# Kernel optimization log

Hardware: AMD Instinct MI355X
Metric: run time of the kernel (lower is better)

Reference implementation:

```python
import jax, jax.numpy as jnp
import numpy as np
from jax import lax

DIM = 128
HEADS = 8
HEAD_DIM = DIM // HEADS
SR = 2
B, H, W = 2, 80, 80
SCALE = HEAD_DIM ** (-0.5)
BN_EPS = 1e-5


def _conv1x1(x, w, b):
    # x: (B,C,H,W), w: (O,C), b: (O,)
    return jnp.einsum('bchw,oc->bohw', x, w) + b[None, :, None, None]


def setup_inputs() -> dict:
    key = jax.random.key(0)
    ks = jax.random.split(key, 12)
    s = DIM ** -0.5
    x = jax.random.normal(ks[0], (B, DIM, H, W), dtype=jnp.float32)
    q_w = jax.random.normal(ks[1], (DIM, DIM), dtype=jnp.float32) * s
    q_b = jnp.zeros((DIM,), jnp.float32)
    k_w = jax.random.normal(ks[2], (DIM, DIM), dtype=jnp.float32) * s
    k_b = jnp.zeros((DIM,), jnp.float32)
    v_w = jax.random.normal(ks[3], (DIM, DIM), dtype=jnp.float32) * s
    v_b = jnp.zeros((DIM,), jnp.float32)
    sr_w = jax.random.normal(ks[4], (DIM, DIM, SR, SR), dtype=jnp.float32) * (s / SR)
    sr_b = jnp.zeros((DIM,), jnp.float32)
    bn_gamma = jnp.ones((DIM,), jnp.float32)
    bn_beta = jnp.zeros((DIM,), jnp.float32)
    bn_mean = jnp.zeros((DIM,), jnp.float32)
    bn_var = jnp.ones((DIM,), jnp.float32)
    proj_w = jax.random.normal(ks[5], (DIM, DIM), dtype=jnp.float32) * s
    proj_b = jnp.zeros((DIM,), jnp.float32)
    return dict(x=x, q_w=q_w, q_b=q_b, k_w=k_w, k_b=k_b, v_w=v_w, v_b=v_b,
                sr_w=sr_w, sr_b=sr_b, bn_gamma=bn_gamma, bn_beta=bn_beta,
                bn_mean=bn_mean, bn_var=bn_var, proj_w=proj_w, proj_b=proj_b)


def reference(x, q_w, q_b, k_w, k_b, v_w, v_b, sr_w, sr_b,
              bn_gamma, bn_beta, bn_mean, bn_var, proj_w, proj_b):
    b, c, h, w = x.shape
    n = h * w
    # q: (B,h,N,d)
    q = _conv1x1(x, q_w, q_b).reshape(b, HEADS, HEAD_DIM, n).transpose(0, 1, 3, 2)
    # spatial reduction: Conv2d(k=SR, s=SR) + BN(eval) + ReLU
    x_kv = lax.conv_general_dilated(x, sr_w, window_strides=(SR, SR),
                                    padding='VALID',
                                    dimension_numbers=('NCHW', 'OIHW', 'NCHW'))
    x_kv = x_kv + sr_b[None, :, None, None]
    inv = bn_gamma / jnp.sqrt(bn_var + BN_EPS)
    x_kv = x_kv * inv[None, :, None, None] + (bn_beta - bn_mean * inv)[None, :, None, None]
    x_kv = jax.nn.relu(x_kv)
    n_kv = x_kv.shape[2] * x_kv.shape[3]
    k = _conv1x1(x_kv, k_w, k_b).reshape(b, HEADS, HEAD_DIM, n_kv).transpose(0, 1, 3, 2)
    v = _conv1x1(x_kv, v_w, v_b).reshape(b, HEADS, HEAD_DIM, n_kv).transpose(0, 1, 3, 2)
    # explicit attention: (B,h,N,N_kv)
    attn = jnp.einsum('bhnd,bhmd->bhnm', q, k) * SCALE
    attn = jax.nn.softmax(attn, axis=-1)
    out = jnp.einsum('bhnm,bhmd->bhnd', attn, v)  # (B,h,N,d)
    # faithful to source layout: transpose(1,2) then reshape to (B,C,H,W)
    out = out.transpose(0, 2, 1, 3).reshape(b, c, h, w)
    out = _conv1x1(out, proj_w, proj_b)
    return out
```

## Files before the change

kernel.cpp:

```cpp
#include <hip/hip_runtime.h>
#include <hip/hip_bf16.h>
#include <cmath>

#define DIM 128
#define HEADS 8
#define NBATCH 2
#define NQ 6400
#define NKV 1600
#define NC 50
#define NSPLIT 5
#define CPS 10
#define BN_EPS 1e-5f
#define LOG2E 1.4426950408889634f

typedef __bf16 bf16_t;
typedef __attribute__((ext_vector_type(8))) __bf16 bf16x8;
typedef __attribute__((ext_vector_type(16))) float f32x16;

union BF8U { bf16x8 v; unsigned u[4]; };

__device__ inline unsigned packbf2(float a, float b) {
  union { __hip_bfloat162 v; unsigned u; } r;
  r.v = __float22bfloat162_rn(make_float2(a, b));
  return r.u;
}

__device__ inline unsigned short f2bf(float v) {
  unsigned u = __float_as_uint(v);
  return (unsigned short)((u + 0x7FFFu + ((u >> 16) & 1u)) >> 16);
}

__global__ __launch_bounds__(256) void wcast(
    const float* __restrict__ qw, const float* __restrict__ kw,
    const float* __restrict__ vw, const float* __restrict__ pw,
    const float* __restrict__ srw, unsigned short* __restrict__ Wb)
{
  int e4 = (blockIdx.x * 256 + threadIdx.x) * 4;
  const float* src; int idx;
  if (e4 < 16384)      { src = qw;  idx = e4; }
  else if (e4 < 32768) { src = kw;  idx = e4 - 16384; }
  else if (e4 < 49152) { src = vw;  idx = e4 - 32768; }
  else if (e4 < 65536) { src = pw;  idx = e4 - 49152; }
  else                 { src = srw; idx = e4 - 65536; }
  float4 v = *(const float4*)(src + idx);
  uint2 wv;
  wv.x = packbf2(v.x, v.y);
  wv.y = packbf2(v.z, v.w);
  *(uint2*)&Wb[e4] = wv;
}

__global__ __launch_bounds__(256) void mgemm_qsrkv(
    const float* __restrict__ x, const bf16_t* __restrict__ Wb,
    const float* __restrict__ q_b, const float* __restrict__ sr_b,
    const float* __restrict__ k_b, const float* __restrict__ v_b,
    const float* __restrict__ bng, const float* __restrict__ bnb,
    const float* __restrict__ bnm, const float* __restrict__ bnv,
    unsigned short* __restrict__ Qb,
    unsigned short* __restrict__ Kp, unsigned short* __restrict__ Vp,
    float sl)
{
  __shared__ __align__(16) unsigned short xs4[32][520];
  __shared__ __align__(16) unsigned short xs[32][136];
  int t = threadIdx.x;
  int ln = t & 31, hf = (t >> 5) & 1, wid = t >> 6;
  int b = blockIdx.y;
  int o = wid * 32 + ln;

  if (blockIdx.x < 50) {
    int cid = blockIdx.x;
    int s0 = cid * 32;

    {
      int tx = t & 31, g = t >> 5;
      int s = s0 + tx;
      int i = s / 40, j = s % 40;
      const float* xb = x + (size_t)b * DIM * NQ;
#pragma unroll
      for (int u = 0; u < 32; ++u) {
        int idx2 = g * 32 + u;
        int c = idx2 >> 1, ky = idx2 & 1;
        const float* src = xb + (size_t)c * NQ + (2 * i + ky) * 80 + 2 * j;
        float2 vv = *(const float2*)src;
        *(unsigned*)&xs4[tx][c * 4 + ky * 2] = packbf2(vv.x, vv.y);
      }
    }
    __syncthreads();

    const unsigned short* arow = &xs4[ln][hf * 8];
    const bf16_t* brow = &Wb[65536 + (size_t)o * 512 + hf * 8];
    f32x16 acc = {};
#pragma unroll 8
    for (int c0 = 0; c0 < 512; c0 += 16) {
      bf16x8 af = *(const bf16x8*)&arow[c0];
      bf16x8 bf = *(const bf16x8*)&brow[c0];
      acc = __builtin_amdgcn_mfma_f32_32x32x16_bf16(af, bf, acc, 0, 0, 0);
    }
    float bv = sr_b[o];
    float inv = bng[o] / sqrtf(bnv[o] + BN_EPS);
    float b2 = bnb[o] - bnm[o] * inv;
#pragma unroll
    for (int g = 0; g < 4; ++g)
#pragma unroll
      for (int jj = 0; jj < 4; ++jj) {
        int sr = 8 * g + 4 * hf + jj;
        xs[sr][o] = f2bf(fmaxf((acc[4 * g + jj] + bv) * inv + b2, 0.f));
      }
    __syncthreads();

    const unsigned short* ar2 = &xs[ln][hf * 8];
    const bf16_t* kbrow = &Wb[16384 + (size_t)o * DIM + hf * 8];
    const bf16_t* vbrow = &Wb[32768 + (size_t)o * DIM + hf * 8];
    f32x16 ka = {}, va = {};
#pragma unroll
    for (int c0 = 0; c0 < 128; c0 += 16) {
      bf16x8 af = *(const bf16x8*)&ar2[c0];
      bf16x8 kb = *(const bf16x8*)&kbrow[c0];
      bf16x8 vb = *(const bf16x8*)&vbrow[c0];
      ka = __builtin_amdgcn_mfma_f32_32x32x16_bf16(af, kb, ka, 0, 0, 0);
      va = __builtin_amdgcn_mfma_f32_32x32x16_bf16(af, vb, va, 0, 0, 0);
    }
    int hloc = o >> 4, d = o & 15;
    {
      float kb2 = k_b[o];
      size_t CB = (((size_t)b * HEADS + hloc) * NC + cid) * 512;
#pragma unroll
      for (int g = 0; g < 4; ++g)
#pragma unroll
        for (int jj = 0; jj < 4; ++jj) {
          int sl2 = 8 * g + 4 * hf + jj;
          Kp[CB + sl2 * 16 + d] = f2bf(ka[4 * g + jj] + kb2);
        }
    }
    {
      float vb2 = v_b[o];
      size_t CB = (((size_t)b * HEADS + hloc) * NC + cid) * 1024;
      uint4 w0, w1;
      w0.x = packbf2(va[0] + vb2, va[1] + vb2);
      w0.y = packbf2(va[2] + vb2, va[3] + vb2);
      w0.z = packbf2(va[4] + vb2, va[5] + vb2);
      w0.w = packbf2(va[6] + vb2, va[7] + vb2);
      w1.x = packbf2(va[8] + vb2, va[9] + vb2);
      w1.y = packbf2(va[10] + vb2, va[11] + vb2);
      w1.z = packbf2(va[12] + vb2, va[13] + vb2);
      w1.w = packbf2(va[14] + vb2, va[15] + vb2);
      *(uint4*)&Vp[CB + d * 16 + hf * 8] = w0;
      *(uint4*)&Vp[CB + 512 + d * 16 + hf * 8] = w1;
    }
    {
      int hh = t >> 5, pos = t & 31;
      size_t addr = (((size_t)b * HEADS + hh) * NC + cid) * 1024 + 256 +
                    ((pos & 16) ? 512 : 0) + (pos & 15);
      Vp[addr] = 0x3F80;
    }
  } else {
    int s0 = (blockIdx.x - 50) * 32;

    {
      int tx = t & 31, cg = t >> 5;
      const float* xb = x + (size_t)b * DIM * NQ + s0 + tx;
#pragma unroll
      for (int it = 0; it < 8; ++it) {
        int c = 2 * cg + 16 * it;
        float a0 = xb[(size_t)c * NQ];
        float a1 = xb[(size_t)(c + 1) * NQ];
        *(unsigned*)&xs[tx][c] = packbf2(a0, a1);
      }
    }
    __syncthreads();

    const unsigned short* arow = &xs[ln][hf * 8];
    const bf16_t* brow = &Wb[(size_t)o * DIM + hf * 8];
    f32x16 acc = {};
#pragma unroll
    for (int c0 = 0; c0 < 128; c0 += 16) {
      bf16x8 af = *(const bf16x8*)&arow[c0];
      bf16x8 bf = *(const bf16x8*)&brow[c0];
      acc = __builtin_amdgcn_mfma_f32_32x32x16_bf16(af, bf, acc, 0, 0, 0);
    }
    float bv = q_b[o];
#pragma unroll
    for (int g = 0; g < 4; ++g)
#pragma unroll
      for (int jj = 0; jj < 4; ++jj) {
        int sq = s0 + 8 * g + 4 * hf + jj;
        Qb[((size_t)b * NQ + sq) * DIM + o] = f2bf((acc[4 * g + jj] + bv) * sl);
      }
  }
}

__global__ __launch_bounds__(256) void attn_split(
    const bf16_t* __restrict__ Qb, const bf16_t* __restrict__ Kp,
    const bf16_t* __restrict__ Vp, unsigned short* __restrict__ Pb,
    float* __restrict__ Lsum)
{
  const int t = threadIdx.x;
  const int ln = t & 31, hf = (t >> 5) & 1, wid = t >> 6;
  const int h = blockIdx.y;
  const int b = blockIdx.z & 1, sp = blockIdx.z >> 1;
  const int q0 = blockIdx.x * 256 + wid * 32;
  const int q1 = q0 + 128;

  bf16x8 qfA = *(const bf16x8*)&Qb[((size_t)b * NQ + q0 + ln) * DIM + h * 16 + hf * 8];
  bf16x8 qfB = *(const bf16x8*)&Qb[((size_t)b * NQ + q1 + ln) * DIM + h * 16 + hf * 8];
  const int bh = b * HEADS + h;
  const bf16_t* kc = &Kp[((size_t)bh * NC + sp * CPS) * 512 + ln * 16 + hf * 8];
  const bf16_t* vc = &Vp[((size_t)bh * NC + sp * CPS) * 1024 + ln * 16 + hf * 8];

  f32x16 aA0 = {}, aA1 = {}, aB0 = {}, aB1 = {};
  const f32x16 zero = {};

  bf16x8 kf0 = *(const bf16x8*)kc;
  bf16x8 va0 = *(const bf16x8*)vc;
  bf16x8 vb0 = *(const bf16x8*)(vc + 512);
  bf16x8 kf1 = *(const bf16x8*)(kc + 512);
  bf16x8 va1 = *(const bf16x8*)(vc + 1024);
  bf16x8 vb1 = *(const bf16x8*)(vc + 1536);

  f32x16 S0a = __builtin_amdgcn_mfma_f32_32x32x16_bf16(kf0, qfA, zero, 0, 0, 0);
  f32x16 S0b = __builtin_amdgcn_mfma_f32_32x32x16_bf16(kf0, qfB, zero, 0, 0, 0);

  for (int c = 0; c < CPS; ++c) {
    int cn = (c + 2 < CPS) ? c + 2 : CPS - 1;
    bf16x8 kf2 = *(const bf16x8*)(kc + (size_t)cn * 512);
    bf16x8 va2 = *(const bf16x8*)(vc + (size_t)cn * 1024);
    bf16x8 vb2 = *(const bf16x8*)(vc + (size_t)cn * 1024 + 512);

    f32x16 S1a = __builtin_amdgcn_mfma_f32_32x32x16_bf16(kf1, qfA, zero, 0, 0, 0);
    f32x16 S1b = __builtin_amdgcn_mfma_f32_32x32x16_bf16(kf1, qfB, zero, 0, 0, 0);

    {
      BF8U f0, f1;
#pragma unroll
      for (int i = 0; i < 4; ++i) {
        f0.u[i] = packbf2(__builtin_amdgcn_exp2f(S0a[2 * i]),
                          __builtin_amdgcn_exp2f(S0a[2 * i + 1]));
        f1.u[i] = packbf2(__builtin_amdgcn_exp2f(S0a[8 + 2 * i]),
                          __builtin_amdgcn_exp2f(S0a[9 + 2 * i]));
      }
      aA0 = __builtin_amdgcn_mfma_f32_32x32x16_bf16(va0, f0.v, aA0, 0, 0, 0);
      aA1 = __builtin_amdgcn_mfma_f32_32x32x16_bf16(vb0, f1.v, aA1, 0, 0, 0);
    }
    {
      BF8U f0, f1;
#pragma unroll
      for (int i = 0; i < 4; ++i) {
        f0.u[i] = packbf2(__builtin_amdgcn_exp2f(S0b[2 * i]),
                          __builtin_amdgcn_exp2f(S0b[2 * i + 1]));
        f1.u[i] = packbf2(__builtin_amdgcn_exp2f(S0b[8 + 2 * i]),
                          __builtin_amdgcn_exp2f(S0b[9 + 2 * i]));
      }
      aB0 = __builtin_amdgcn_mfma_f32_32x32x16_bf16(va0, f0.v, aB0, 0, 0, 0);
      aB1 = __builtin_amdgcn_mfma_f32_32x32x16_bf16(vb0, f1.v, aB1, 0, 0, 0);
    }

    S0a = S1a; S0b = S1b;
    kf0 = kf1; va0 = va1; vb0 = vb1;
    kf1 = kf2; va1 = va2; vb1 = vb2;
  }

  f32x16 accA, accB;
#pragma unroll
  for (int i = 0; i < 16; ++i) { accA[i] = aA0[i] + aA1[i]; accB[i] = aB0[i] + aB1[i]; }

  size_t sbase = (size_t)(sp * 2 + b) * (NQ * DIM);
  {
    unsigned short* prow = &Pb[sbase + (size_t)(q0 + ln) * DIM + h * 16 + 4 * hf];
    uint2 w0, w1;
    w0.x = packbf2(accA[0], accA[1]); w0.y = packbf2(accA[2], accA[3]);
    w1.x = packbf2(accA[4], accA[5]); w1.y = packbf2(accA[6], accA[7]);
    *(uint2*)&prow[0] = w0;
    *(uint2*)&prow[8] = w1;
  }
  {
    unsigned short* prow = &Pb[sbase + (size_t)(q1 + ln) * DIM + h * 16 + 4 * hf];
    uint2 w0, w1;
    w0.x = packbf2(accB[0], accB[1]); w0.y = packbf2(accB[2], accB[3]);
    w1.x = packbf2(accB[4], accB[5]); w1.y = packbf2(accB[6], accB[7]);
    *(uint2*)&prow[0] = w0;
    *(uint2*)&prow[8] = w1;
  }
  if (!hf) {
    size_t lbase = (size_t)(sp * 2 + b) * (HEADS * NQ) + (size_t)h * NQ;
    Lsum[lbase + q0 + ln] = accA[8];
    Lsum[lbase + q1 + ln] = accB[8];
  }
}

__global__ __launch_bounds__(256) void proj_comb(
    const unsigned short* __restrict__ Pb, const float* __restrict__ Lsum,
    const bf16_t* __restrict__ Wb, const float* __restrict__ p_b,
    float* __restrict__ Out)
{
  __shared__ __align__(16) unsigned short As[32][136];
  int t = threadIdx.x;
  int b = blockIdx.y;
  int s0 = blockIdx.x * 32;

  {
    int tp = t & 15, cg = t >> 4;
#pragma unroll
    for (int it = 0; it < 8; ++it) {
      int c = cg * 8 + it;
      int f = c * NQ + s0 + 2 * tp;
      int n = f >> 7, hh = (f >> 4) & 7;
      float plo = 0.f, phi = 0.f, L = 0.f;
#pragma unroll
      for (int s = 0; s < NSPLIT; ++s) {
        unsigned u = *(const unsigned*)&Pb[(size_t)(2 * s + b) * (NQ * DIM) + f];
        plo += __uint_as_float(u << 16);
        phi += __uint_as_float(u & 0xFFFF0000u);
        L += Lsum[(size_t)(2 * s + b) * (HEADS * NQ) + (size_t)hh * NQ + n];
      }
      As[2 * tp][c]     = f2bf(plo / L);
      As[2 * tp + 1][c] = f2bf(phi / L);
    }
  }
  __syncthreads();

  int ln = t & 31, hf = (t >> 5) & 1, wid = t >> 6;
  int o = wid * 32 + ln;
  const bf16_t* brow = &Wb[49152 + (size_t)o * DIM + hf * 8];
  const unsigned short* arow = &As[ln][hf * 8];
  f32x16 acc = {};
#pragma unroll
  for (int c0 = 0; c0 < 128; c0 += 16) {
    bf16x8 af = *(const bf16x8*)&arow[c0];
    bf16x8 bf = *(const bf16x8*)&brow[c0];
    acc = __builtin_amdgcn_mfma_f32_32x32x16_bf16(af, bf, acc, 0, 0, 0);
  }
  float bv = p_b[o];
  float* obase = &Out[((size_t)b * DIM + o) * NQ + s0 + 4 * hf];
#pragma unroll
  for (int g = 0; g < 4; ++g) {
    float4 r;
    r.x = acc[4 * g + 0] + bv; r.y = acc[4 * g + 1] + bv;
    r.z = acc[4 * g + 2] + bv; r.w = acc[4 * g + 3] + bv;
    *(float4*)&obase[8 * g] = r;
  }
}

extern "C" void kernel_launch(void* const* d_in, const int* in_sizes, int n_in,
                              void* d_out, int out_size, void* d_ws, size_t ws_size,
                              hipStream_t stream)
{
  const float* x    = (const float*)d_in[0];
  const float* q_w  = (const float*)d_in[1];
  const float* q_b  = (const float*)d_in[2];
  const float* k_w  = (const float*)d_in[3];
  const float* k_b  = (const float*)d_in[4];
  const float* v_w  = (const float*)d_in[5];
  const float* v_b  = (const float*)d_in[6];
  const float* sr_w = (const float*)d_in[7];
  const float* sr_b = (const float*)d_in[8];
  const float* bng  = (const float*)d_in[9];
  const float* bnb  = (const float*)d_in[10];
  const float* bnm  = (const float*)d_in[11];
  const float* bnv  = (const float*)d_in[12];
  const float* p_w  = (const float*)d_in[13];
  const float* p_b  = (const float*)d_in[14];
  float* out = (float*)d_out;

  float* ws = (float*)d_ws;
  bf16_t* Qb   = (bf16_t*)(ws);
  bf16_t* Kp   = (bf16_t*)(ws + 819200);
  bf16_t* Vp   = (bf16_t*)(ws + 1024000);
  float*  Lsum = ws + 1433600;
  bf16_t* Pb   = (bf16_t*)(ws + 1945600);
  bf16_t* Wb   = (bf16_t*)(ws + 6041600);

  const float sl = 0.25f * LOG2E;

  wcast<<<dim3(128), dim3(256), 0, stream>>>(
      q_w, k_w, v_w, p_w, sr_w, (unsigned short*)Wb);

  mgemm_qsrkv<<<dim3(250, NBATCH), dim3(256), 0, stream>>>(
      x, Wb, q_b, sr_b, k_b, v_b, bng, bnb, bnm, bnv,
      (unsigned short*)Qb, (unsigned short*)Kp, (unsigned short*)Vp, sl);

  attn_split<<<dim3(NQ / 256, HEADS, 2 * NSPLIT), dim3(256), 0, stream>>>(
      Qb, Kp, Vp, (unsigned short*)Pb, Lsum);

  proj_comb<<<dim3(200, NBATCH), dim3(256), 0, stream>>>(
      (const unsigned short*)Pb, Lsum, Wb, p_b, out);
}
```

Measured before the change: 143.7 us.

## Stage K/V chunks in double-buffered LDS and reduce KV split count

```diff
diff --git a/kernel.cpp b/kernel.cpp
--- a/kernel.cpp
+++ b/kernel.cpp
@@ -8,8 +8,8 @@
 #define NQ 6400
 #define NKV 1600
 #define NC 50
-#define NSPLIT 5
-#define CPS 10
+#define NSPLIT 2
+#define CPS 25
 #define BN_EPS 1e-5f
 #define LOG2E 1.4426950408889634f
 
@@ -193,97 +193,72 @@
     const bf16_t* __restrict__ Vp, unsigned short* __restrict__ Pb,
     float* __restrict__ Lsum)
 {
+  __shared__ __align__(16) unsigned short ldsK[2][512];
+  __shared__ __align__(16) unsigned short ldsV[2][1024];
+
   const int t = threadIdx.x;
   const int ln = t & 31, hf = (t >> 5) & 1, wid = t >> 6;
   const int h = blockIdx.y;
   const int b = blockIdx.z & 1, sp = blockIdx.z >> 1;
-  const int q0 = blockIdx.x * 256 + wid * 32;
-  const int q1 = q0 + 128;
-
-  bf16x8 qfA = *(const bf16x8*)&Qb[((size_t)b * NQ + q0 + ln) * DIM + h * 16 + hf * 8];
-  bf16x8 qfB = *(const bf16x8*)&Qb[((size_t)b * NQ + q1 + ln) * DIM + h * 16 + hf * 8];
+  const int q0 = blockIdx.x * 128 + wid * 32;
+
+  bf16x8 qf = *(const bf16x8*)&Qb[((size_t)b * NQ + q0 + ln) * DIM + h * 16 + hf * 8];
   const int bh = b * HEADS + h;
-  const bf16_t* kc = &Kp[((size_t)bh * NC + sp * CPS) * 512 + ln * 16 + hf * 8];
-  const bf16_t* vc = &Vp[((size_t)bh * NC + sp * CPS) * 1024 + ln * 16 + hf * 8];
-
-  f32x16 aA0 = {}, aA1 = {}, aB0 = {}, aB1 = {};
+  const bf16_t* kcg = &Kp[((size_t)bh * NC + sp * CPS) * 512];
+  const bf16_t* vcg = &Vp[((size_t)bh * NC + sp * CPS) * 1024];
+
+  if (t < 64)       *(uint4*)&ldsK[0][t * 8] = *(const uint4*)&kcg[t * 8];
+  else if (t < 192) *(uint4*)&ldsV[0][(t - 64) * 8] = *(const uint4*)&vcg[(t - 64) * 8];
+  __syncthreads();
+
+  f32x16 acc0 = {}, acc1 = {};
   const f32x16 zero = {};
 
-  bf16x8 kf0 = *(const bf16x8*)kc;
-  bf16x8 va0 = *(const bf16x8*)vc;
-  bf16x8 vb0 = *(const bf16x8*)(vc + 512);
-  bf16x8 kf1 = *(const bf16x8*)(kc + 512);
-  bf16x8 va1 = *(const bf16x8*)(vc + 1024);
-  bf16x8 vb1 = *(const bf16x8*)(vc + 1536);
-
-  f32x16 S0a = __builtin_amdgcn_mfma_f32_32x32x16_bf16(kf0, qfA, zero, 0, 0, 0);
-  f32x16 S0b = __builtin_amdgcn_mfma_f32_32x32x16_bf16(kf0, qfB, zero, 0, 0, 0);
-
   for (int c = 0; c < CPS; ++c) {
-    int cn = (c + 2 < CPS) ? c + 2 : CPS - 1;
-    bf16x8 kf2 = *(const bf16x8*)(kc + (size_t)cn * 512);
-    bf16x8 va2 = *(const bf16x8*)(vc + (size_t)cn * 1024);
-    bf16x8 vb2 = *(const bf16x8*)(vc + (size_t)cn * 1024 + 512);
-
-    f32x16 S1a = __builtin_amdgcn_mfma_f32_32x32x16_bf16(kf1, qfA, zero, 0, 0, 0);
-    f32x16 S1b = __builtin_amdgcn_mfma_f32_32x32x16_bf16(kf1, qfB, zero, 0, 0, 0);
-
-    {
-      BF8U f0, f1;
-#pragma unroll
-      for (int i = 0; i < 4; ++i) {
-        f0.u[i] = packbf2(__builtin_amdgcn_exp2f(S0a[2 * i]),
-                          __builtin_amdgcn_exp2f(S0a[2 * i + 1]));
-        f1.u[i] = packbf2(__builtin_amdgcn_exp2f(S0a[8 + 2 * i]),
-                          __builtin_amdgcn_exp2f(S0a[9 + 2 * i]));
-      }
-      aA0 = __builtin_amdgcn_mfma_f32_32x32x16_bf16(va0, f0.v, aA0, 0, 0, 0);
-      aA1 = __builtin_amdgcn_mfma_f32_32x32x16_bf16(vb0, f1.v, aA1, 0, 0, 0);
-    }
-    {
-      BF8U f0, f1;
-#pragma unroll
-      for (int i = 0; i < 4; ++i) {
-        f0.u[i] = packbf2(__builtin_amdgcn_exp2f(S0b[2 * i]),
-                          __builtin_amdgcn_exp2f(S0b[2 * i + 1]));
-        f1.u[i] = packbf2(__builtin_amdgcn_exp2f(S0b[8 + 2 * i]),
-                          __builtin_amdgcn_exp2f(S0b[9 + 2 * i]));
-      }
-      aB0 = __builtin_amdgcn_mfma_f32_32x32x16_bf16(va0, f0.v, aB0, 0, 0, 0);
-      aB1 = __builtin_amdgcn_mfma_f32_32x32x16_bf16(vb0, f1.v, aB1, 0, 0, 0);
-    }
-
-    S0a = S1a; S0b = S1b;
-    kf0 = kf1; va0 = va1; vb0 = vb1;
-    kf1 = kf2; va1 = va2; vb1 = vb2;
-  }
-
-  f32x16 accA, accB;
-#pragma unroll
-  for (int i = 0; i < 16; ++i) { accA[i] = aA0[i] + aA1[i]; accB[i] = aB0[i] + aB1[i]; }
-
-  size_t sbase = (size_t)(sp * 2 + b) * (NQ * DIM);
-  {
-    unsigned short* prow = &Pb[sbase + (size_t)(q0 + ln) * DIM + h * 16 + 4 * hf];
-    uint2 w0, w1;
-    w0.x = packbf2(accA[0], accA[1]); w0.y = packbf2(accA[2], accA[3]);
-    w1.x = packbf2(accA[4], accA[5]); w1.y = packbf2(accA[6], accA[7]);
-    *(uint2*)&prow[0] = w0;
-    *(uint2*)&prow[8] = w1;
-  }
-  {
-    unsigned short* prow = &Pb[sbase + (size_t)(q1 + ln) * DIM + h * 16 + 4 * hf];
-    uint2 w0, w1;
-    w0.x = packbf2(accB[0], accB[1]); w0.y = packbf2(accB[2], accB[3]);
-    w1.x = packbf2(accB[4], accB[5]); w1.y = packbf2(accB[6], accB[7]);
-    *(uint2*)&prow[0] = w0;
-    *(uint2*)&prow[8] = w1;
-  }
-  if (!hf) {
-    size_t lbase = (size_t)(sp * 2 + b) * (HEADS * NQ) + (size_t)h * NQ;
-    Lsum[lbase + q0 + ln] = accA[8];
-    Lsum[lbase + q1 + ln] = accB[8];
-  }
+    const int cb = c & 1;
+    uint4 tmp;
+    if (c + 1 < CPS) {
+      if (t < 64)       tmp = *(const uint4*)&kcg[(size_t)(c + 1) * 512 + t * 8];
+      else if (t < 192) tmp = *(const uint4*)&vcg[(size_t)(c + 1) * 1024 + (t - 64) * 8];
+    }
+
+    bf16x8 kf = *(const bf16x8*)&ldsK[cb][ln * 16 + hf * 8];
+    f32x16 S = __builtin_amdgcn_mfma_f32_32x32x16_bf16(kf, qf, zero, 0, 0, 0);
+
+    BF8U f0, f1;
+#pragma unroll
+    for (int i = 0; i < 4; ++i) {
+      f0.u[i] = packbf2(__builtin_amdgcn_exp2f(S[2 * i]),
+                        __builtin_amdgcn_exp2f(S[2 * i + 1]));
+      f1.u[i] = packbf2(__builtin_amdgcn_exp2f(S[8 + 2 * i]),
+                        __builtin_amdgcn_exp2f(S[9 + 2 * i]));
+    }
+
+    bf16x8 va = *(const bf16x8*)&ldsV[cb][ln * 16 + hf * 8];
+    bf16x8 vb = *(const bf16x8*)&ldsV[cb][512 + ln * 16 + hf * 8];
+    acc0 = __builtin_amdgcn_mfma_f32_32x32x16_bf16(va, f0.v, acc0, 0, 0, 0);
+    acc1 = __builtin_amdgcn_mfma_f32_32x32x16_bf16(vb, f1.v, acc1, 0, 0, 0);
+
+    if (c + 1 < CPS) {
+      if (t < 64)       *(uint4*)&ldsK[cb ^ 1][t * 8] = tmp;
+      else if (t < 192) *(uint4*)&ldsV[cb ^ 1][(t - 64) * 8] = tmp;
+    }
+    __syncthreads();
+  }
+
+  f32x16 acc;
+#pragma unroll
+  for (int i = 0; i < 16; ++i) acc[i] = acc0[i] + acc1[i];
+
+  unsigned short* prow =
+      &Pb[(size_t)(sp * 2 + b) * (NQ * DIM) + (size_t)(q0 + ln) * DIM + h * 16 + 4 * hf];
+  uint2 w0, w1;
+  w0.x = packbf2(acc[0], acc[1]); w0.y = packbf2(acc[2], acc[3]);
+  w1.x = packbf2(acc[4], acc[5]); w1.y = packbf2(acc[6], acc[7]);
+  *(uint2*)&prow[0] = w0;
+  *(uint2*)&prow[8] = w1;
+  if (!hf)
+    Lsum[(size_t)(sp * 2 + b) * (HEADS * NQ) + (size_t)h * NQ + q0 + ln] = acc[8];
 }
 
 __global__ __launch_bounds__(256) void proj_comb(
@@ -377,7 +352,7 @@
       x, Wb, q_b, sr_b, k_b, v_b, bng, bnb, bnm, bnv,
       (unsigned short*)Qb, (unsigned short*)Kp, (unsigned short*)Vp, sl);
 
-  attn_split<<<dim3(NQ / 256, HEADS, 2 * NSPLIT), dim3(256), 0, stream>>>(
+  attn_split<<<dim3(NQ / 128, HEADS, 2 * NSPLIT), dim3(256), 0, stream>>>(
       Qb, Kp, Vp, (unsigned short*)Pb, Lsum);
 
   proj_comb<<<dim3(200, NBATCH), dim3(256), 0, stream>>>(
```

Measured after the change: 156.9 us. 1.09x slower.
